# Optimization experiments

Measured on AMD Instinct MI355X. Metric: run time of the kernel, lower is better.

## Reference

```python
import jax, jax.numpy as jnp
import numpy as np

NB_OBJ = 3
DIM_BODY = 10
DIM_OBJ = 15
DIM_LEMB = 100
PHI_IN = DIM_LEMB + DIM_BODY + 2 * (NB_OBJ + DIM_OBJ)  # 146
HID = 256
PHI_OUT = 256
ACT_DIM = 4
BATCH = 65536
LOG_SIG_MIN, LOG_SIG_MAX = -20.0, 2.0
# permutations of 3 objects taken 2: (0,1),(0,2),(1,0),(1,2),(2,0),(2,1)
IDX_I = np.array([0, 0, 1, 1, 2, 2])
IDX_J = np.array([1, 2, 0, 2, 0, 1])


def _xavier(key, fan_in, fan_out):
    lim = float(np.sqrt(6.0 / (fan_in + fan_out)))
    return jax.random.uniform(key, (fan_in, fan_out), jnp.float32, -lim, lim)


def setup_inputs() -> dict:
    key = jax.random.key(0)
    ks = jax.random.split(key, 8)
    return {
        "obs": jax.random.normal(ks[0], (BATCH, DIM_BODY + NB_OBJ * DIM_OBJ), jnp.float32),
        "l_emb": jax.random.normal(ks[1], (BATCH, DIM_LEMB), jnp.float32),
        "phi_w1": _xavier(ks[2], PHI_IN, HID), "phi_b1": jnp.zeros((HID,), jnp.float32),
        "phi_w2": _xavier(ks[3], HID, PHI_OUT), "phi_b2": jnp.zeros((PHI_OUT,), jnp.float32),
        "rho_w1": _xavier(ks[4], PHI_OUT, HID), "rho_b1": jnp.zeros((HID,), jnp.float32),
        "mean_w": _xavier(ks[5], HID, ACT_DIM), "mean_b": jnp.zeros((ACT_DIM,), jnp.float32),
        "lstd_w": _xavier(ks[6], HID, ACT_DIM), "lstd_b": jnp.zeros((ACT_DIM,), jnp.float32),
    }


def reference(obs, l_emb, phi_w1, phi_b1, phi_w2, phi_b2,
              rho_w1, rho_b1, mean_w, mean_b, lstd_w, lstd_b):
    B = obs.shape[0]
    obs_body = obs[:, :DIM_BODY]                                   # [B, 10]
    obj_feats = obs[:, DIM_BODY:].reshape(B, NB_OBJ, DIM_OBJ)      # [B, 3, 15]
    one_hot = jnp.broadcast_to(jnp.eye(NB_OBJ, dtype=obs.dtype)[None], (B, NB_OBJ, NB_OBJ))
    objs = jnp.concatenate([one_hot, obj_feats], axis=-1)          # [B, 3, 18]
    base = jnp.concatenate([l_emb, obs_body], axis=-1)             # [B, 110]
    # pairwise concat over the 6 ordered pairs -> [6, B, 146]
    xi = objs[:, IDX_I].transpose(1, 0, 2)                         # [6, B, 18]
    xj = objs[:, IDX_J].transpose(1, 0, 2)
    base6 = jnp.broadcast_to(base[None], (6, B, base.shape[-1]))
    inp = jnp.concatenate([base6, xi, xj], axis=-1)                # [6, B, 146]
    # phi MLP
    h = jax.nn.relu(jnp.einsum('pbi,ih->pbh', inp, phi_w1) + phi_b1)
    h = jax.nn.relu(jnp.einsum('pbh,ho->pbo', h, phi_w2) + phi_b2)
    agg = h.sum(axis=0)                                            # [B, 256]
    # rho MLP
    r = jax.nn.relu(agg @ rho_w1 + rho_b1)
    mean = r @ mean_w + mean_b
    log_std = jnp.clip(r @ lstd_w + lstd_b, LOG_SIG_MIN, LOG_SIG_MAX)
    return mean, log_std
```

## Files before the change

### kernel.cpp

```cpp
#include <hip/hip_runtime.h>

#define BATCH 65536
#define TB 16

typedef _Float16 half8 __attribute__((ext_vector_type(8)));
typedef _Float16 half2v __attribute__((ext_vector_type(2)));
typedef float fx4 __attribute__((ext_vector_type(4)));

#define PW1B_OFF 0
#define PW1F_OFF 32768
#define PW2_OFF  40960
#define PWR_OFF  106496
#define PWH_OFF  172032
#define WS_TOTAL 176128

#define HIDX(row, col) (((((col) >> 5) * 4 + (((col) >> 3) & 3)) * 16 + (row)) * 8 + ((col) & 7))

__global__ __launch_bounds__(256) void prep_weights(
    const float* __restrict__ w1, const float* __restrict__ w2,
    const float* __restrict__ wr, const float* __restrict__ wm,
    const float* __restrict__ wl, _Float16* __restrict__ ws)
{
  int idx = blockIdx.x * 256 + threadIdx.x;
  if (idx < 32768) {
    int kk = idx & 31, n = (idx >> 5) & 255, kt = idx >> 13;
    int k = kt * 32 + kk;
    ws[idx] = (k < 110) ? (_Float16)w1[k * 256 + n] : (_Float16)0.f;
  } else if (idx < 40960) {
    int t = idx - 32768;
    int kk = t & 31, n = t >> 5;
    _Float16 v = (_Float16)0.f;
    if (kk < 15)                  v = (_Float16)w1[(113 + kk) * 256 + n];
    else if (kk >= 16 && kk < 31) v = (_Float16)w1[(131 + (kk - 16)) * 256 + n];
    ws[idx] = v;
  } else if (idx < 106496) {
    int t = idx - 40960;
    int kk = t & 31, n = (t >> 5) & 255, kt = t >> 13;
    ws[idx] = (_Float16)w2[(kt * 32 + kk) * 256 + n];
  } else if (idx < 172032) {
    int t = idx - 106496;
    int kk = t & 31, n = (t >> 5) & 255, kt = t >> 13;
    ws[idx] = (_Float16)wr[(kt * 32 + kk) * 256 + n];
  } else if (idx < WS_TOTAL) {
    int t = idx - 172032;
    int kk = t & 31, n = (t >> 5) & 15, kt = t >> 9;
    int k = kt * 32 + kk;
    _Float16 v = (_Float16)0.f;
    if (n < 4) v = (_Float16)wm[k * 4 + n];
    else if (n < 8) v = (_Float16)wl[k * 4 + (n - 4)];
    ws[PWH_OFF + t] = v;
  }
}

__global__ __launch_bounds__(512) void actor_fused(
    const float* __restrict__ obs, const float* __restrict__ lemb,
    const float* __restrict__ w1, const _Float16* __restrict__ ws,
    const float* __restrict__ b1, const float* __restrict__ b2,
    const float* __restrict__ br, const float* __restrict__ bm,
    const float* __restrict__ bl, float* __restrict__ out)
{
  __shared__ __align__(16) _Float16 H1[6 * 16 * 256];
  __shared__ __align__(16) _Float16 Bb[16 * 256];
  __shared__ __align__(16) _Float16 Os[3 * 16 * 16];
  __shared__ __align__(16) _Float16 Bs[6 * 256];

  const _Float16* __restrict__ pw1b = ws + PW1B_OFF;
  const _Float16* __restrict__ pw1f = ws + PW1F_OFF;
  const _Float16* __restrict__ pw2  = ws + PW2_OFF;
  const _Float16* __restrict__ pwr  = ws + PWR_OFF;
  const _Float16* __restrict__ pwh  = ws + PWH_OFF;

  const int tid  = threadIdx.x;
  const int wave = tid >> 6;
  const int lane = tid & 63;
  const int q    = lane >> 4;
  const int l16  = lane & 15;
  const int colbase = wave * 32;
  const int rowbase = blockIdx.x * TB;

  for (int idx = tid; idx < 1024; idx += 512) {
    int r = idx >> 6, c2 = idx & 63, c = c2 * 2;
    float v0 = 0.f, v1 = 0.f;
    if (c2 < 50) {
      float2 v = ((const float2*)(lemb + (rowbase + r) * 100))[c2];
      v0 = v.x; v1 = v.y;
    } else if (c < 110) {
      v0 = obs[(rowbase + r) * 55 + (c - 100)];
      v1 = (c + 1 < 110) ? obs[(rowbase + r) * 55 + (c - 99)] : 0.f;
    }
    half2v hv = {(_Float16)v0, (_Float16)v1};
    *(half2v*)&Bb[HIDX(r, c)] = hv;
  }
  for (int idx = tid; idx < 768; idx += 512) {
    int o = idx >> 8, rem = idx & 255, r = rem >> 4, c = rem & 15;
    float v = (c < 15) ? obs[(rowbase + r) * 55 + 10 + o * 15 + c] : 0.f;
    Os[o * 256 + ((c >> 3) * 16 + r) * 8 + (c & 7)] = (_Float16)v;
  }
  for (int idx = tid; idx < 1536; idx += 512) {
    int p = idx >> 8, c = idx & 255;
    int oi = p >> 1, oj = (1161 >> (2 * p)) & 3;
    Bs[idx] = (_Float16)(b1[c] + w1[(110 + oi) * 256 + c] + w1[(128 + oj) * 256 + c]);
  }
  __syncthreads();

  const fx4 zero4 = {0.f, 0.f, 0.f, 0.f};

  fx4 u[2];
  u[0] = zero4; u[1] = zero4;
  #pragma unroll 2
  for (int kt = 0; kt < 4; ++kt) {
    half8 a = *(const half8*)&Bb[((kt * 4 + q) * 16 + l16) * 8];
    #pragma unroll
    for (int nt = 0; nt < 2; ++nt) {
      half8 b = *(const half8*)&pw1b[(kt * 256 + colbase + nt * 16 + l16) * 32 + q * 8];
      u[nt] = __builtin_amdgcn_mfma_f32_16x16x32_f16(a, b, u[nt], 0, 0, 0);
    }
  }

  half8 b1f[2];
  #pragma unroll
  for (int nt = 0; nt < 2; ++nt)
    b1f[nt] = *(const half8*)&pw1f[(colbase + nt * 16 + l16) * 32 + q * 8];

  #pragma unroll
  for (int p = 0; p < 6; ++p) {
    const int oi = p >> 1;
    const int oj = (1161 >> (2 * p)) & 3;
    const int o = (q < 2) ? oi : oj;
    half8 af = *(const half8*)&Os[o * 256 + ((q & 1) * 16 + l16) * 8];
    #pragma unroll
    for (int nt = 0; nt < 2; ++nt) {
      int col = colbase + nt * 16 + l16;
      fx4 acc1 = __builtin_amdgcn_mfma_f32_16x16x32_f16(af, b1f[nt], u[nt], 0, 0, 0);
      float bs = (float)Bs[p * 256 + col];
      #pragma unroll
      for (int rr = 0; rr < 4; ++rr) {
        float h = acc1[rr] + bs;
        H1[p * 4096 + HIDX(q * 4 + rr, col)] = (_Float16)(h > 0.f ? h : 0.f);
      }
    }
  }
  __syncthreads();

  float bsg[2];
  bsg[0] = b2[colbase + l16];
  bsg[1] = b2[colbase + 16 + l16];
  fx4 acc[12];
  #pragma unroll
  for (int i = 0; i < 12; ++i) {
    float bs = bsg[i & 1];
    acc[i][0] = bs; acc[i][1] = bs; acc[i][2] = bs; acc[i][3] = bs;
  }
  #pragma unroll 2
  for (int kt = 0; kt < 8; ++kt) {
    half8 a[6];
    #pragma unroll
    for (int p = 0; p < 6; ++p)
      a[p] = *(const half8*)&H1[p * 4096 + ((kt * 4 + q) * 16 + l16) * 8];
    #pragma unroll
    for (int nt = 0; nt < 2; ++nt) {
      half8 b = *(const half8*)&pw2[(kt * 256 + colbase + nt * 16 + l16) * 32 + q * 8];
      #pragma unroll
      for (int p = 0; p < 6; ++p)
        acc[p * 2 + nt] = __builtin_amdgcn_mfma_f32_16x16x32_f16(a[p], b, acc[p * 2 + nt], 0, 0, 0);
    }
  }
  #pragma unroll
  for (int nt = 0; nt < 2; ++nt) {
    fx4 agg = zero4;
    #pragma unroll
    for (int p = 0; p < 6; ++p)
      #pragma unroll
      for (int rr = 0; rr < 4; ++rr) {
        float h = acc[p * 2 + nt][rr];
        if (h > 0.f) agg[rr] += h;
      }
    int col = colbase + nt * 16 + l16;
    #pragma unroll
    for (int rr = 0; rr < 4; ++rr)
      Bb[HIDX(q * 4 + rr, col)] = (_Float16)agg[rr];
  }
  __syncthreads();

  float bsr0 = br[colbase + l16];
  float bsr1 = br[colbase + 16 + l16];
  fx4 acc3[2];
  acc3[0][0] = bsr0; acc3[0][1] = bsr0; acc3[0][2] = bsr0; acc3[0][3] = bsr0;
  acc3[1][0] = bsr1; acc3[1][1] = bsr1; acc3[1][2] = bsr1; acc3[1][3] = bsr1;
  #pragma unroll 2
  for (int kt = 0; kt < 8; ++kt) {
    half8 a = *(const half8*)&Bb[((kt * 4 + q) * 16 + l16) * 8];
    #pragma unroll
    for (int nt = 0; nt < 2; ++nt) {
      half8 b = *(const half8*)&pwr[(kt * 256 + colbase + nt * 16 + l16) * 32 + q * 8];
      acc3[nt] = __builtin_amdgcn_mfma_f32_16x16x32_f16(a, b, acc3[nt], 0, 0, 0);
    }
  }
  #pragma unroll
  for (int nt = 0; nt < 2; ++nt) {
    int col = colbase + nt * 16 + l16;
    #pragma unroll
    for (int rr = 0; rr < 4; ++rr) {
      float h = acc3[nt][rr];
      H1[HIDX(q * 4 + rr, col)] = (_Float16)(h > 0.f ? h : 0.f);
    }
  }
  __syncthreads();

  if (wave == 0) {
    fx4 a4 = zero4;
    for (int kt = 0; kt < 8; ++kt) {
      half8 a = *(const half8*)&H1[((kt * 4 + q) * 16 + l16) * 8];
      half8 b = *(const half8*)&pwh[(kt * 16 + l16) * 32 + q * 8];
      a4 = __builtin_amdgcn_mfma_f32_16x16x32_f16(a, b, a4, 0, 0, 0);
    }
    int gr = rowbase + q * 4;
    if (l16 < 4) {
      float bias = bm[l16];
      #pragma unroll
      for (int rr = 0; rr < 4; ++rr) out[(gr + rr) * 4 + l16] = a4[rr] + bias;
    } else if (l16 < 8) {
      int c = l16 - 4;
      float bias = bl[c];
      #pragma unroll
      for (int rr = 0; rr < 4; ++rr) {
        float v = a4[rr] + bias;
        v = v < -20.f ? -20.f : (v > 2.f ? 2.f : v);
        out[BATCH * 4 + (gr + rr) * 4 + c] = v;
      }
    }
  }
}

extern "C" void kernel_launch(void* const* d_in, const int* in_sizes, int n_in,
                              void* d_out, int out_size, void* d_ws, size_t ws_size,
                              hipStream_t stream) {
  const float* obs  = (const float*)d_in[0];
  const float* lemb = (const float*)d_in[1];
  const float* w1   = (const float*)d_in[2];
  const float* b1   = (const float*)d_in[3];
  const float* w2   = (const float*)d_in[4];
  const float* b2   = (const float*)d_in[5];
  const float* wr   = (const float*)d_in[6];
  const float* br   = (const float*)d_in[7];
  const float* wm   = (const float*)d_in[8];
  const float* bm   = (const float*)d_in[9];
  const float* wl   = (const float*)d_in[10];
  const float* bl   = (const float*)d_in[11];
  float* out = (float*)d_out;
  _Float16* ws = (_Float16*)d_ws;

  hipLaunchKernelGGL(prep_weights, dim3(WS_TOTAL / 256), dim3(256), 0, stream,
                     w1, w2, wr, wm, wl, ws);
  hipLaunchKernelGGL(actor_fused, dim3(BATCH / TB), dim3(512), 0, stream,
                     obs, lemb, w1, (const _Float16*)ws, b1, b2, br, bm, bl, out);
}
```

Measured before the change: 201.9 us.

## Process 32 rows per block with swapped MFMA operands and two-phase pair grouping

```diff
diff --git a/kernel.cpp b/kernel.cpp
--- a/kernel.cpp
+++ b/kernel.cpp
@@ -1,9 +1,10 @@
 #include <hip/hip_runtime.h>
 
 #define BATCH 65536
-#define TB 16
+#define TB 32
 
 typedef _Float16 half8 __attribute__((ext_vector_type(8)));
+typedef _Float16 half4v __attribute__((ext_vector_type(4)));
 typedef _Float16 half2v __attribute__((ext_vector_type(2)));
 typedef float fx4 __attribute__((ext_vector_type(4)));
 
@@ -13,8 +14,6 @@
 #define PWR_OFF  106496
 #define PWH_OFF  172032
 #define WS_TOTAL 176128
-
-#define HIDX(row, col) (((((col) >> 5) * 4 + (((col) >> 3) & 3)) * 16 + (row)) * 8 + ((col) & 7))
 
 __global__ __launch_bounds__(256) void prep_weights(
     const float* __restrict__ w1, const float* __restrict__ w2,
@@ -52,7 +51,7 @@
   }
 }
 
-__global__ __launch_bounds__(512) void actor_fused(
+__global__ __launch_bounds__(512, 4) void actor_fused(
     const float* __restrict__ obs, const float* __restrict__ lemb,
     const float* __restrict__ w1, const _Float16* __restrict__ ws,
     const float* __restrict__ b1, const float* __restrict__ b2,
@@ -60,9 +59,9 @@
     const float* __restrict__ bl, float* __restrict__ out)
 {
   __shared__ __align__(16) _Float16 H1[6 * 16 * 256];
-  __shared__ __align__(16) _Float16 Bb[16 * 256];
-  __shared__ __align__(16) _Float16 Os[3 * 16 * 16];
-  __shared__ __align__(16) _Float16 Bs[6 * 256];
+  __shared__ __align__(16) _Float16 Bb[32 * 256];
+  __shared__ __align__(16) _Float16 Os[3 * 32 * 16];
+  __shared__ __align__(16) float    Bsf[6 * 256];
 
   const _Float16* __restrict__ pw1b = ws + PW1B_OFF;
   const _Float16* __restrict__ pw1f = ws + PW1F_OFF;
@@ -78,7 +77,10 @@
   const int colbase = wave * 32;
   const int rowbase = blockIdx.x * TB;
 
-  for (int idx = tid; idx < 1024; idx += 512) {
+  const int c0_0 = colbase + q * 4;
+  const int c0_1 = colbase + 16 + q * 4;
+
+  for (int idx = tid; idx < 2048; idx += 512) {
     int r = idx >> 6, c2 = idx & 63, c = c2 * 2;
     float v0 = 0.f, v1 = 0.f;
     if (c2 < 50) {
@@ -89,145 +91,166 @@
       v1 = (c + 1 < 110) ? obs[(rowbase + r) * 55 + (c - 99)] : 0.f;
     }
     half2v hv = {(_Float16)v0, (_Float16)v1};
-    *(half2v*)&Bb[HIDX(r, c)] = hv;
-  }
-  for (int idx = tid; idx < 768; idx += 512) {
-    int o = idx >> 8, rem = idx & 255, r = rem >> 4, c = rem & 15;
-    float v = (c < 15) ? obs[(rowbase + r) * 55 + 10 + o * 15 + c] : 0.f;
-    Os[o * 256 + ((c >> 3) * 16 + r) * 8 + (c & 7)] = (_Float16)v;
+    *(half2v*)&Bb[((c >> 3) * 32 + r) * 8 + (c & 7)] = hv;
+  }
+  for (int idx = tid; idx < 1536; idx += 512) {
+    int o = idx >> 9, rem = idx & 511, r = rem >> 4, k = rem & 15;
+    float v = (k < 15) ? obs[(rowbase + r) * 55 + 10 + o * 15 + k] : 0.f;
+    Os[o * 512 + ((k >> 3) * 32 + r) * 8 + (k & 7)] = (_Float16)v;
   }
   for (int idx = tid; idx < 1536; idx += 512) {
     int p = idx >> 8, c = idx & 255;
     int oi = p >> 1, oj = (1161 >> (2 * p)) & 3;
-    Bs[idx] = (_Float16)(b1[c] + w1[(110 + oi) * 256 + c] + w1[(128 + oj) * 256 + c]);
+    Bsf[idx] = b1[c] + w1[(110 + oi) * 256 + c] + w1[(128 + oj) * 256 + c];
   }
   __syncthreads();
 
   const fx4 zero4 = {0.f, 0.f, 0.f, 0.f};
 
-  fx4 u[2];
-  u[0] = zero4; u[1] = zero4;
-  #pragma unroll 2
+  fx4 u[4];
+  u[0] = zero4; u[1] = zero4; u[2] = zero4; u[3] = zero4;
+  #pragma unroll
   for (int kt = 0; kt < 4; ++kt) {
-    half8 a = *(const half8*)&Bb[((kt * 4 + q) * 16 + l16) * 8];
+    half8 a0 = *(const half8*)&Bb[((kt * 4 + q) * 32 + l16) * 8];
+    half8 a1 = *(const half8*)&Bb[((kt * 4 + q) * 32 + 16 + l16) * 8];
     #pragma unroll
     for (int nt = 0; nt < 2; ++nt) {
       half8 b = *(const half8*)&pw1b[(kt * 256 + colbase + nt * 16 + l16) * 32 + q * 8];
-      u[nt] = __builtin_amdgcn_mfma_f32_16x16x32_f16(a, b, u[nt], 0, 0, 0);
-    }
-  }
-
-  half8 b1f[2];
+      u[nt]     = __builtin_amdgcn_mfma_f32_16x16x32_f16(b, a0, u[nt], 0, 0, 0);
+      u[2 + nt] = __builtin_amdgcn_mfma_f32_16x16x32_f16(b, a1, u[2 + nt], 0, 0, 0);
+    }
+  }
+
+  auto g1_group = [&](int g) {
+    half8 b1f0 = *(const half8*)&pw1f[(colbase + l16) * 32 + q * 8];
+    half8 b1f1 = *(const half8*)&pw1f[(colbase + 16 + l16) * 32 + q * 8];
+    #pragma unroll
+    for (int pp = 0; pp < 3; ++pp) {
+      const int p = g * 3 + pp;
+      const int oi = p >> 1, oj = (1161 >> (2 * p)) & 3;
+      const int o = (q < 2) ? oi : oj;
+      #pragma unroll
+      for (int rt = 0; rt < 2; ++rt) {
+        half8 af = *(const half8*)&Os[o * 512 + ((q & 1) * 32 + rt * 16 + l16) * 8];
+        #pragma unroll
+        for (int nt = 0; nt < 2; ++nt) {
+          fx4 t = __builtin_amdgcn_mfma_f32_16x16x32_f16(nt ? b1f1 : b1f0, af,
+                                                         u[rt * 2 + nt], 0, 0, 0);
+          const int c0 = nt ? c0_1 : c0_0;
+          fx4 bs = *(const fx4*)&Bsf[p * 256 + c0];
+          float h0 = fmaxf(t[0] + bs[0], 0.f);
+          float h1v = fmaxf(t[1] + bs[1], 0.f);
+          float h2v = fmaxf(t[2] + bs[2], 0.f);
+          float h3v = fmaxf(t[3] + bs[3], 0.f);
+          half4v hv = {(_Float16)h0, (_Float16)h1v, (_Float16)h2v, (_Float16)h3v};
+          *(half4v*)&H1[(pp * 2 + rt) * 4096 + ((c0 >> 3) * 16 + l16) * 8 + (c0 & 7)] = hv;
+        }
+      }
+    }
+  };
+
+  fx4 agg[4];
+  agg[0] = zero4; agg[1] = zero4; agg[2] = zero4; agg[3] = zero4;
+  fx4 b2v[2];
+  b2v[0] = *(const fx4*)&b2[c0_0];
+  b2v[1] = *(const fx4*)&b2[c0_1];
+
+  auto g2_group = [&]() {
+    fx4 acc[12];
+    #pragma unroll
+    for (int i = 0; i < 12; ++i) acc[i] = b2v[i & 1];
+    #pragma unroll 2
+    for (int kt = 0; kt < 8; ++kt) {
+      half8 bb0 = *(const half8*)&pw2[(kt * 256 + colbase + l16) * 32 + q * 8];
+      half8 bb1 = *(const half8*)&pw2[(kt * 256 + colbase + 16 + l16) * 32 + q * 8];
+      #pragma unroll
+      for (int t6 = 0; t6 < 6; ++t6) {
+        half8 a = *(const half8*)&H1[t6 * 4096 + ((kt * 4 + q) * 16 + l16) * 8];
+        acc[t6 * 2]     = __builtin_amdgcn_mfma_f32_16x16x32_f16(bb0, a, acc[t6 * 2], 0, 0, 0);
+        acc[t6 * 2 + 1] = __builtin_amdgcn_mfma_f32_16x16x32_f16(bb1, a, acc[t6 * 2 + 1], 0, 0, 0);
+      }
+    }
+    #pragma unroll
+    for (int t6 = 0; t6 < 6; ++t6)
+      #pragma unroll
+      for (int nt = 0; nt < 2; ++nt)
+        #pragma unroll
+        for (int rr = 0; rr < 4; ++rr) {
+          float h = acc[t6 * 2 + nt][rr];
+          if (h > 0.f) agg[(t6 & 1) * 2 + nt][rr] += h;
+        }
+  };
+
+  g1_group(0);
+  __syncthreads();
+  g2_group();
+  __syncthreads();
+  g1_group(1);
+  __syncthreads();
+  g2_group();
+
   #pragma unroll
-  for (int nt = 0; nt < 2; ++nt)
-    b1f[nt] = *(const half8*)&pw1f[(colbase + nt * 16 + l16) * 32 + q * 8];
-
-  #pragma unroll
-  for (int p = 0; p < 6; ++p) {
-    const int oi = p >> 1;
-    const int oj = (1161 >> (2 * p)) & 3;
-    const int o = (q < 2) ? oi : oj;
-    half8 af = *(const half8*)&Os[o * 256 + ((q & 1) * 16 + l16) * 8];
-    #pragma unroll
-    for (int nt = 0; nt < 2; ++nt) {
-      int col = colbase + nt * 16 + l16;
-      fx4 acc1 = __builtin_amdgcn_mfma_f32_16x16x32_f16(af, b1f[nt], u[nt], 0, 0, 0);
-      float bs = (float)Bs[p * 256 + col];
-      #pragma unroll
-      for (int rr = 0; rr < 4; ++rr) {
-        float h = acc1[rr] + bs;
-        H1[p * 4096 + HIDX(q * 4 + rr, col)] = (_Float16)(h > 0.f ? h : 0.f);
-      }
-    }
-  }
-  __syncthreads();
-
-  float bsg[2];
-  bsg[0] = b2[colbase + l16];
-  bsg[1] = b2[colbase + 16 + l16];
-  fx4 acc[12];
-  #pragma unroll
-  for (int i = 0; i < 12; ++i) {
-    float bs = bsg[i & 1];
-    acc[i][0] = bs; acc[i][1] = bs; acc[i][2] = bs; acc[i][3] = bs;
+  for (int rt = 0; rt < 2; ++rt)
+    #pragma unroll
+    for (int nt = 0; nt < 2; ++nt) {
+      const int c0 = nt ? c0_1 : c0_0;
+      fx4 t = agg[rt * 2 + nt];
+      half4v hv = {(_Float16)t[0], (_Float16)t[1], (_Float16)t[2], (_Float16)t[3]};
+      *(half4v*)&Bb[((c0 >> 3) * 32 + rt * 16 + l16) * 8 + (c0 & 7)] = hv;
+    }
+  __syncthreads();
+
+  fx4 acc3[4];
+  {
+    fx4 brv0 = *(const fx4*)&br[c0_0];
+    fx4 brv1 = *(const fx4*)&br[c0_1];
+    acc3[0] = brv0; acc3[1] = brv1; acc3[2] = brv0; acc3[3] = brv1;
   }
   #pragma unroll 2
   for (int kt = 0; kt < 8; ++kt) {
-    half8 a[6];
-    #pragma unroll
-    for (int p = 0; p < 6; ++p)
-      a[p] = *(const half8*)&H1[p * 4096 + ((kt * 4 + q) * 16 + l16) * 8];
-    #pragma unroll
-    for (int nt = 0; nt < 2; ++nt) {
-      half8 b = *(const half8*)&pw2[(kt * 256 + colbase + nt * 16 + l16) * 32 + q * 8];
-      #pragma unroll
-      for (int p = 0; p < 6; ++p)
-        acc[p * 2 + nt] = __builtin_amdgcn_mfma_f32_16x16x32_f16(a[p], b, acc[p * 2 + nt], 0, 0, 0);
+    half8 a0 = *(const half8*)&Bb[((kt * 4 + q) * 32 + l16) * 8];
+    half8 a1 = *(const half8*)&Bb[((kt * 4 + q) * 32 + 16 + l16) * 8];
+    #pragma unroll
+    for (int nt = 0; nt < 2; ++nt) {
+      half8 b = *(const half8*)&pwr[(kt * 256 + colbase + nt * 16 + l16) * 32 + q * 8];
+      acc3[nt]     = __builtin_amdgcn_mfma_f32_16x16x32_f16(b, a0, acc3[nt], 0, 0, 0);
+      acc3[2 + nt] = __builtin_amdgcn_mfma_f32_16x16x32_f16(b, a1, acc3[2 + nt], 0, 0, 0);
     }
   }
   #pragma unroll
-  for (int nt = 0; nt < 2; ++nt) {
-    fx4 agg = zero4;
-    #pragma unroll
-    for (int p = 0; p < 6; ++p)
+  for (int rt = 0; rt < 2; ++rt)
+    #pragma unroll
+    for (int nt = 0; nt < 2; ++nt) {
+      const int c0 = nt ? c0_1 : c0_0;
+      fx4 t = acc3[rt * 2 + nt];
+      half4v hv = {(_Float16)fmaxf(t[0], 0.f), (_Float16)fmaxf(t[1], 0.f),
+                   (_Float16)fmaxf(t[2], 0.f), (_Float16)fmaxf(t[3], 0.f)};
+      *(half4v*)&H1[rt * 4096 + ((c0 >> 3) * 16 + l16) * 8 + (c0 & 7)] = hv;
+    }
+  __syncthreads();
+
+  if (wave < 2) {
+    fx4 a4 = zero4;
+    #pragma unroll 2
+    for (int kt = 0; kt < 8; ++kt) {
+      half8 rfrag = *(const half8*)&H1[wave * 4096 + ((kt * 4 + q) * 16 + l16) * 8];
+      half8 wfrag = *(const half8*)&pwh[(kt * 16 + l16) * 32 + q * 8];
+      a4 = __builtin_amdgcn_mfma_f32_16x16x32_f16(wfrag, rfrag, a4, 0, 0, 0);
+    }
+    const int row = rowbase + wave * 16 + l16;
+    if (q == 0) {
+      fx4 bm4 = *(const fx4*)bm;
+      fx4 o = {a4[0] + bm4[0], a4[1] + bm4[1], a4[2] + bm4[2], a4[3] + bm4[3]};
+      *(fx4*)&out[row * 4] = o;
+    } else if (q == 1) {
+      fx4 bl4 = *(const fx4*)bl;
+      fx4 o;
       #pragma unroll
       for (int rr = 0; rr < 4; ++rr) {
-        float h = acc[p * 2 + nt][rr];
-        if (h > 0.f) agg[rr] += h;
+        float v = a4[rr] + bl4[rr];
+        o[rr] = v < -20.f ? -20.f : (v > 2.f ? 2.f : v);
       }
-    int col = colbase + nt * 16 + l16;
-    #pragma unroll
-    for (int rr = 0; rr < 4; ++rr)
-      Bb[HIDX(q * 4 + rr, col)] = (_Float16)agg[rr];
-  }
-  __syncthreads();
-
-  float bsr0 = br[colbase + l16];
-  float bsr1 = br[colbase + 16 + l16];
-  fx4 acc3[2];
-  acc3[0][0] = bsr0; acc3[0][1] = bsr0; acc3[0][2] = bsr0; acc3[0][3] = bsr0;
-  acc3[1][0] = bsr1; acc3[1][1] = bsr1; acc3[1][2] = bsr1; acc3[1][3] = bsr1;
-  #pragma unroll 2
-  for (int kt = 0; kt < 8; ++kt) {
-    half8 a = *(const half8*)&Bb[((kt * 4 + q) * 16 + l16) * 8];
-    #pragma unroll
-    for (int nt = 0; nt < 2; ++nt) {
-      half8 b = *(const half8*)&pwr[(kt * 256 + colbase + nt * 16 + l16) * 32 + q * 8];
-      acc3[nt] = __builtin_amdgcn_mfma_f32_16x16x32_f16(a, b, acc3[nt], 0, 0, 0);
-    }
-  }
-  #pragma unroll
-  for (int nt = 0; nt < 2; ++nt) {
-    int col = colbase + nt * 16 + l16;
-    #pragma unroll
-    for (int rr = 0; rr < 4; ++rr) {
-      float h = acc3[nt][rr];
-      H1[HIDX(q * 4 + rr, col)] = (_Float16)(h > 0.f ? h : 0.f);
-    }
-  }
-  __syncthreads();
-
-  if (wave == 0) {
-    fx4 a4 = zero4;
-    for (int kt = 0; kt < 8; ++kt) {
-      half8 a = *(const half8*)&H1[((kt * 4 + q) * 16 + l16) * 8];
-      half8 b = *(const half8*)&pwh[(kt * 16 + l16) * 32 + q * 8];
-      a4 = __builtin_amdgcn_mfma_f32_16x16x32_f16(a, b, a4, 0, 0, 0);
-    }
-    int gr = rowbase + q * 4;
-    if (l16 < 4) {
-      float bias = bm[l16];
-      #pragma unroll
-      for (int rr = 0; rr < 4; ++rr) out[(gr + rr) * 4 + l16] = a4[rr] + bias;
-    } else if (l16 < 8) {
-      int c = l16 - 4;
-      float bias = bl[c];
-      #pragma unroll
-      for (int rr = 0; rr < 4; ++rr) {
-        float v = a4[rr] + bias;
-        v = v < -20.f ? -20.f : (v > 2.f ? 2.f : v);
-        out[BATCH * 4 + (gr + rr) * 4 + c] = v;
-      }
+      *(fx4*)&out[BATCH * 4 + row * 4] = o;
     }
   }
 }
```

Result: faster. 189.1 us (-6.3%).
